# Kernel optimization log

Measured on AMD Instinct MI355X. Metric: run time of the kernel, lower is better.

Reference implementation:

```python
import jax, jax.numpy as jnp
import numpy as np

N = 100000
E = 1600000
D_IN = 128
D_HID = 32
NEG_SLOPE = 0.2


def _glorot(key, shape):
    fan_in, fan_out = shape[0], shape[-1]
    lim = jnp.sqrt(6.0 / (fan_in + fan_out))
    return jax.random.uniform(key, shape, jnp.float32, -lim, lim)


def setup_inputs() -> dict:
    key = jax.random.key(0)
    ks = jax.random.split(key, 10)
    x = jax.random.normal(ks[0], (N, D_IN), jnp.float32)
    edge_index = jax.random.randint(ks[1], (2, E), 0, N, jnp.int64)
    return {
        "x": x,
        "edge_index": edge_index,
        "W1_l": _glorot(ks[2], (D_IN, D_HID)),
        "W1_r": _glorot(ks[3], (D_IN, D_HID)),
        "att1": _glorot(ks[4], (D_HID,)),
        "b1": jnp.zeros((D_HID,), jnp.float32),
        "W2_l": _glorot(ks[5], (D_HID, D_HID)),
        "W2_r": _glorot(ks[6], (D_HID, D_HID)),
        "att2": _glorot(ks[7], (D_HID,)),
        "b2": jnp.zeros((D_HID,), jnp.float32),
    }


def _segment_softmax(logits, seg, num_segments):
    m = jax.ops.segment_max(logits, seg, num_segments=num_segments)
    m = jnp.where(jnp.isfinite(m), m, 0.0)
    ex = jnp.exp(logits - m[seg])
    s = jax.ops.segment_sum(ex, seg, num_segments=num_segments)
    return ex / (s[seg] + 1e-16)


def _gatv2(x, edge_index, W_l, W_r, att, b):
    # GATv2Conv, heads=1, add_self_loops=False, share_weights=False
    src, dst = edge_index[0], edge_index[1]
    x_l = x @ W_l  # source transform [N, D_HID]
    x_r = x @ W_r  # target transform [N, D_HID]
    # per-edge attention logit: att . leaky_relu(x_l[j] + x_r[i])
    h = x_l[src] + x_r[dst]  # [E, D_HID]
    e = jnp.where(h > 0, h, NEG_SLOPE * h) @ att  # [E]
    alpha = _segment_softmax(e, dst, x.shape[0])  # softmax over incoming edges
    out = jax.ops.segment_sum(alpha[:, None] * x_l[src], dst,
                              num_segments=x.shape[0])
    return out + b


def reference(x, edge_index, W1_l, W1_r, att1, b1, W2_l, W2_r, att2, b2):
    h = _gatv2(x, edge_index, W1_l, W1_r, att1, b1)
    h = jax.nn.relu(h)
    return _gatv2(h, edge_index, W2_l, W2_r, att2, b2)
```

## Files before the change

kernel.cpp:

```cpp
#include <hip/hip_runtime.h>
#include <hip/hip_bf16.h>

#define D_HID 32
#define D_IN 128
#define NEG 0.2f
#define BSH 7
#define BSZ 128
#define MAXB 1024
#define SCATB 256

typedef unsigned short u16;
typedef __attribute__((ext_vector_type(8))) short short8;
typedef __attribute__((ext_vector_type(4))) float float4v;

__device__ __forceinline__ float b2f(u16 u){
  union { unsigned int i; float f; } c; c.i = ((unsigned int)u) << 16; return c.f;
}

__device__ __forceinline__ u16 f2b_rne(float f){
  union { float f; unsigned int u; } c; c.f = f;
  unsigned int u = c.u;
  return (u16)((u + 0x7FFFu + ((u >> 16) & 1u)) >> 16);
}

__device__ __forceinline__ void split_bf16(float v, u16& hi, u16& lo){
  hi = f2b_rne(v);
  lo = f2b_rne(v - b2f(hi));
}

__device__ __forceinline__ float ldf(const void* __restrict__ p, int f32, long long i){
  return f32 ? ((const float*)p)[i] : b2f(((const u16*)p)[i]);
}

__device__ __forceinline__ int atomAddI(int* p, int v){
  return __hip_atomic_fetch_add(p, v, __ATOMIC_RELAXED, __HIP_MEMORY_SCOPE_AGENT);
}

__device__ __forceinline__ float red8(float p){
  p += __int_as_float(__builtin_amdgcn_update_dpp(
         0, __float_as_int(p), 0xB1, 0xF, 0xF, true));
  p += __int_as_float(__builtin_amdgcn_update_dpp(
         0, __float_as_int(p), 0x4E, 0xF, 0xF, true));
  p += __int_as_float(__builtin_amdgcn_ds_swizzle(
         __float_as_int(p), 0x101F));
  return p;
}

__device__ __forceinline__ float edge_ev(const float4 xv, const float4 xrk,
                                         const float4 attk){
  float hx = xv.x + xrk.x; hx = fmaxf(hx, NEG*hx);
  float hy = xv.y + xrk.y; hy = fmaxf(hy, NEG*hy);
  float hz = xv.z + xrk.z; hz = fmaxf(hz, NEG*hz);
  float hw = xv.w + xrk.w; hw = fmaxf(hw, NEG*hw);
  float p = hx*attk.x;
  p = fmaf(hy, attk.y, p);
  p = fmaf(hz, attk.z, p);
  p = fmaf(hw, attk.w, p);
  p = red8(p);
  p = fminf(p, 60.f);
  return __expf(p);
}

__global__ void __launch_bounds__(256)
count_flags(const int* __restrict__ ei, const u16* __restrict__ xw,
            int* __restrict__ gcnt, int* __restrict__ flags, int E_, int B_){
  __shared__ int hist[MAXB];
  __shared__ int nz_s, insane_s;
  int t = threadIdx.x;
  if (t == 0){ nz_s = 0; insane_s = 0; }
  for (int i = t; i < B_; i += 256) hist[i] = 0;
  __syncthreads();
  if (t < 64 && ei[2*t+1] != 0) atomicAdd(&nz_s, 1);
  if (blockIdx.x == 0){
    int e = (xw[t] >> 7) & 0xFF;
    if (e < 100 || e > 140) atomicAdd(&insane_s, 1);
  }
  __syncthreads();
  int is64 = (nz_s == 0);
  if (blockIdx.x == 0 && t == 0){
    flags[0] = is64;
    flags[1] = (insane_s > 16) ? 1 : 0;
  }
  int chunk = (E_ + gridDim.x - 1) / gridDim.x;
  int s = blockIdx.x * chunk;
  int e = s + chunk; if (e > E_) e = E_;
  for (int i = s + t; i < e; i += 256){
    int dst = is64 ? ei[2*E_ + 2*i] : ei[E_ + i];
    atomicAdd(&hist[dst >> BSH], 1);
  }
  __syncthreads();
  for (int i = t; i < B_; i += 256)
    if (hist[i]) (void)atomAddI(&gcnt[i], hist[i]);
}

__device__ __forceinline__ void prep_body(const void* __restrict__ Wl,
                                          const void* __restrict__ Wr,
                                          int f32, int K,
                                          uint4* __restrict__ whi,
                                          uint4* __restrict__ wlo, int t){
  int KS = K >> 5;
  int total = 4 * KS * 64;
  if (t >= total) return;
  int lane = t & 63;
  int rem = t >> 6;
  int kstep = rem % KS;
  int ctile = rem / KS;
  int col = ctile * 16 + (lane & 15);
  int quad = lane >> 4;
  union { u16 s[8]; uint4 q; } ch, cl;
  #pragma unroll
  for (int j = 0; j < 8; ++j){
    int k = kstep*32 + quad*8 + j;
    float v = (col < 32) ? ldf(Wl, f32, (long long)k*D_HID + col)
                         : ldf(Wr, f32, (long long)k*D_HID + (col - 32));
    u16 hi, lo; split_bf16(v, hi, lo);
    ch.s[j] = hi; cl.s[j] = lo;
  }
  whi[rem*64 + lane] = ch.q;
  wlo[rem*64 + lane] = cl.q;
}

__global__ void __launch_bounds__(256)
scan_scatter_prep(const int* __restrict__ ei, const int* __restrict__ flags,
                  const int* __restrict__ gcnt, int* __restrict__ cur0,
                  unsigned* __restrict__ seg, int* __restrict__ offsets,
                  const void* __restrict__ W1l, const void* __restrict__ W1r,
                  const void* __restrict__ W2l, const void* __restrict__ W2r,
                  uint4* __restrict__ whi1, uint4* __restrict__ wlo1,
                  uint4* __restrict__ whi2, uint4* __restrict__ wlo2,
                  int E_, int B_){
  int t = threadIdx.x;
  if ((int)blockIdx.x >= SCATB){
    int sub = blockIdx.x - SCATB;
    int f32 = flags[1];
    if (sub < 4) prep_body(W1l, W1r, f32, D_IN,  whi1, wlo1, sub*256 + t);
    else         prep_body(W2l, W2r, f32, D_HID, whi2, wlo2, t);
    return;
  }
  __shared__ int sd[MAXB];
  __shared__ int part[256];
  __shared__ int hist[MAXB];
  __shared__ int bbase[MAXB];
  for (int i = t; i < MAXB; i += 256) sd[i] = (i < B_) ? gcnt[i] : 0;
  __syncthreads();
  int a0 = sd[4*t], a1 = sd[4*t+1], a2 = sd[4*t+2], a3 = sd[4*t+3];
  int mysum = a0 + a1 + a2 + a3;
  part[t] = mysum;
  __syncthreads();
  for (int off = 1; off < 256; off <<= 1){
    int v = (t >= off) ? part[t-off] : 0;
    __syncthreads();
    part[t] += v;
    __syncthreads();
  }
  int excl = part[t] - mysum;
  sd[4*t]   = excl;
  sd[4*t+1] = excl + a0;
  sd[4*t+2] = excl + a0 + a1;
  sd[4*t+3] = excl + a0 + a1 + a2;
  __syncthreads();
  if (blockIdx.x == 0){
    for (int i = t; i <= B_; i += 256)
      offsets[i] = (i < MAXB) ? sd[i] : part[255];
  }
  for (int i = t; i < B_; i += 256) hist[i] = 0;
  __syncthreads();
  int is64 = flags[0];
  int chunk = (E_ + SCATB - 1) / SCATB;
  int s = blockIdx.x * chunk;
  int e = s + chunk; if (e > E_) e = E_;
  for (int i = s + t; i < e; i += 256){
    int dst = is64 ? ei[2*E_ + 2*i] : ei[E_ + i];
    atomicAdd(&hist[dst >> BSH], 1);
  }
  __syncthreads();
  for (int i = t; i < B_; i += 256){
    int c = hist[i];
    bbase[i] = c ? (sd[i] + atomAddI(&cur0[i], c)) : 0;
  }
  __syncthreads();
  for (int i = t; i < B_; i += 256) hist[i] = 0;
  __syncthreads();
  for (int i = s + t; i < e; i += 256){
    int src, dst;
    if (is64){ src = ei[2*i]; dst = ei[2*E_ + 2*i]; }
    else     { src = ei[i];   dst = ei[E_ + i]; }
    int b = dst >> BSH;
    int pos = bbase[b] + atomicAdd(&hist[b], 1);
    seg[pos] = ((unsigned)src << BSH) | (unsigned)(dst & (BSZ-1));
  }
}

__device__ void finalize_body(const unsigned* __restrict__ seg,
                              const int* __restrict__ offsets,
                              int* __restrict__ row, int* __restrict__ csr_src,
                              int N_, int B_, int b, int t){
  __shared__ int hist[BSZ];
  __shared__ int sc[BSZ];
  __shared__ int loff[BSZ];
  int base = offsets[b], cnt = offsets[b+1] - base;
  if (t < BSZ) hist[t] = 0;
  __syncthreads();
  for (int i = t; i < cnt; i += 256)
    atomicAdd(&hist[seg[base+i] & (BSZ-1)], 1);
  __syncthreads();
  if (t < BSZ) sc[t] = hist[t];
  __syncthreads();
  for (int off = 1; off < BSZ; off <<= 1){
    int tmp = (t < BSZ && t >= off) ? sc[t-off] : 0;
    __syncthreads();
    if (t < BSZ) sc[t] += tmp;
    __syncthreads();
  }
  if (t < BSZ){
    int excl = sc[t] - hist[t];
    loff[t] = excl;
    int node = b*BSZ + t;
    if (node <= N_) row[node] = base + excl;
  }
  if (b == B_-1 && t == 0) row[N_] = offsets[B_];
  __syncthreads();
  for (int i = t; i < cnt; i += 256){
    unsigned en = seg[base+i];
    int dl = en & (BSZ-1);
    int pos = atomicAdd(&loff[dl], 1);
    csr_src[base + pos] = (int)en;
  }
}

template<int K>
__device__ __forceinline__ void gemm_body(const void* __restrict__ X,
                          const uint4* __restrict__ whi, const uint4* __restrict__ wlo,
                          const int* __restrict__ flags, int force_f32,
                          float* __restrict__ xl, float* __restrict__ xr,
                          int N_, int tile, int lane)
{
  constexpr int KS = K >> 5;
  if (tile * 16 >= N_) return;
  int quad = lane >> 4;
  int m = tile*16 + (lane & 15);
  if (m >= N_) m = N_ - 1;
  int f32 = force_f32 | flags[1];

  float4v acc[4];
  #pragma unroll
  for (int c = 0; c < 4; ++c) acc[c] = (float4v){0.f,0.f,0.f,0.f};

  #pragma unroll
  for (int ks = 0; ks < KS; ++ks){
    long long base = (long long)m * K + ks*32 + quad*8;
    float av[8];
    if (f32){
      const float4* xp = (const float4*)((const float*)X + base);
      float4 t0 = xp[0], t1 = xp[1];
      av[0]=t0.x; av[1]=t0.y; av[2]=t0.z; av[3]=t0.w;
      av[4]=t1.x; av[5]=t1.y; av[6]=t1.z; av[7]=t1.w;
    } else {
      union { uint4 q; u16 s[8]; } c8;
      c8.q = *(const uint4*)((const u16*)X + base);
      #pragma unroll
      for (int j = 0; j < 8; ++j) av[j] = b2f(c8.s[j]);
    }
    short8 ahi, alo;
    #pragma unroll
    for (int j = 0; j < 8; ++j){
      u16 hi, lo; split_bf16(av[j], hi, lo);
      ahi[j] = (short)hi; alo[j] = (short)lo;
    }
    #pragma unroll
    for (int c = 0; c < 4; ++c){
      uint4 wh = whi[(c*KS + ks)*64 + lane];
      uint4 wl = wlo[(c*KS + ks)*64 + lane];
      short8 bh = *(short8*)&wh;
      short8 bl = *(short8*)&wl;
      acc[c] = __builtin_amdgcn_mfma_f32_16x16x32_bf16(ahi, bh, acc[c], 0, 0, 0);
      acc[c] = __builtin_amdgcn_mfma_f32_16x16x32_bf16(ahi, bl, acc[c], 0, 0, 0);
      acc[c] = __builtin_amdgcn_mfma_f32_16x16x32_bf16(alo, bh, acc[c], 0, 0, 0);
    }
  }

  #pragma unroll
  for (int c = 0; c < 4; ++c){
    int col = c*16 + (lane & 15);
    float* dst = (col < 32) ? xl : xr;
    int kk = col & 31;
    #pragma unroll
    for (int r = 0; r < 4; ++r){
      int node = tile*16 + quad*4 + r;
      if (node < N_) dst[(size_t)node*D_HID + kk] = acc[c][r];
    }
  }
}

template<int K>
__global__ void __launch_bounds__(256)
fin_gemm(const unsigned* __restrict__ seg, const int* __restrict__ offsets,
         int* __restrict__ row, int* __restrict__ csr_src,
         const void* __restrict__ X,
         const uint4* __restrict__ whi, const uint4* __restrict__ wlo,
         const int* __restrict__ flags,
         float* __restrict__ xl, float* __restrict__ xr, int N_, int B_){
  if ((int)blockIdx.x < B_){
    finalize_body(seg, offsets, row, csr_src, N_, B_, blockIdx.x, threadIdx.x);
    return;
  }
  int tile = (blockIdx.x - B_) * 4 + (threadIdx.x >> 6);
  gemm_body<K>(X, whi, wlo, flags, 0, xl, xr, N_, tile, threadIdx.x & 63);
}

template<int K>
__global__ void __launch_bounds__(256)
mfma_gemm(const void* __restrict__ X,
          const uint4* __restrict__ whi, const uint4* __restrict__ wlo,
          const int* __restrict__ flags, int force_f32,
          float* __restrict__ xl, float* __restrict__ xr, int N_){
  int tile = blockIdx.x * 4 + (threadIdx.x >> 6);
  gemm_body<K>(X, whi, wlo, flags, force_f32, xl, xr, N_, tile, threadIdx.x & 63);
}

__global__ void __launch_bounds__(256)
gat_gather(const int* __restrict__ row, const unsigned* __restrict__ csrp,
           const float* __restrict__ xl, const float* __restrict__ xr,
           const void* __restrict__ att, const void* __restrict__ bias,
           const int* __restrict__ flags,
           float* __restrict__ outp, int N_, int do_relu)
{
  int wv = (blockIdx.x * blockDim.x + threadIdx.x) >> 6;
  int l = threadIdx.x & 63;
  int n = wv * 4 + (l >> 4);
  if (n >= N_) return;
  int half = (l >> 3) & 1;
  int fl = l & 7;
  int f32 = flags[1];
  float4 attk;
  attk.x = ldf(att, f32, fl*4+0);
  attk.y = ldf(att, f32, fl*4+1);
  attk.z = ldf(att, f32, fl*4+2);
  attk.w = ldf(att, f32, fl*4+3);
  float4 xrk = *(const float4*)(xr + (size_t)n*D_HID + fl*4);
  int rs = row[n], re = row[n+1];
  const char* xlb = (const char*)xl;
  unsigned fo = (unsigned)(fl << 4);

  float4 acc = make_float4(0.f, 0.f, 0.f, 0.f);
  float ssum = 0.f;

  int start = rs + 2*half;
  if (start < re){
    int last = re - 1;
    unsigned c0 = csrp[start];
    unsigned c1 = csrp[min(start+1,  last)];
    unsigned c2 = csrp[min(start+4,  last)];
    unsigned c3 = csrp[min(start+5,  last)];
    unsigned c4 = csrp[min(start+8,  last)];
    unsigned c5 = csrp[min(start+9,  last)];
    unsigned ca = csrp[min(start+12, last)];
    unsigned cb = csrp[min(start+13, last)];
    float4 xv0 = *(const float4*)(xlb + (c0 & ~127u) + fo);
    float4 xv1 = *(const float4*)(xlb + (c1 & ~127u) + fo);
    float4 xv2 = *(const float4*)(xlb + (c2 & ~127u) + fo);
    float4 xv3 = *(const float4*)(xlb + (c3 & ~127u) + fo);
    float4 xv4 = *(const float4*)(xlb + (c4 & ~127u) + fo);
    float4 xv5 = *(const float4*)(xlb + (c5 & ~127u) + fo);
    for (int i = start; i < re; i += 4){
      float4 nx0 = *(const float4*)(xlb + (ca & ~127u) + fo);
      float4 nx1 = *(const float4*)(xlb + (cb & ~127u) + fo);
      unsigned na = csrp[min(i+16, last)];
      unsigned nb = csrp[min(i+17, last)];
      float ev0 = edge_ev(xv0, xrk, attk);
      ssum += ev0;
      acc.x = fmaf(ev0, xv0.x, acc.x);
      acc.y = fmaf(ev0, xv0.y, acc.y);
      acc.z = fmaf(ev0, xv0.z, acc.z);
      acc.w = fmaf(ev0, xv0.w, acc.w);
      float ev1 = edge_ev(xv1, xrk, attk);
      ev1 = (i + 1 <= last) ? ev1 : 0.f;
      ssum += ev1;
      acc.x = fmaf(ev1, xv1.x, acc.x);
      acc.y = fmaf(ev1, xv1.y, acc.y);
      acc.z = fmaf(ev1, xv1.z, acc.z);
      acc.w = fmaf(ev1, xv1.w, acc.w);
      xv0 = xv2; xv1 = xv3; xv2 = xv4; xv3 = xv5; xv4 = nx0; xv5 = nx1;
      ca = na; cb = nb;
    }
  }

  acc.x += __shfl_xor(acc.x, 8, 16);
  acc.y += __shfl_xor(acc.y, 8, 16);
  acc.z += __shfl_xor(acc.z, 8, 16);
  acc.w += __shfl_xor(acc.w, 8, 16);
  ssum  += __shfl_xor(ssum,  8, 16);

  if (half == 0){
    float inv = 1.0f / (ssum + 1e-16f);
    float4 o;
    o.x = acc.x*inv + ldf(bias, f32, fl*4+0);
    o.y = acc.y*inv + ldf(bias, f32, fl*4+1);
    o.z = acc.z*inv + ldf(bias, f32, fl*4+2);
    o.w = acc.w*inv + ldf(bias, f32, fl*4+3);
    if (do_relu){
      o.x = fmaxf(o.x, 0.f); o.y = fmaxf(o.y, 0.f);
      o.z = fmaxf(o.z, 0.f); o.w = fmaxf(o.w, 0.f);
    }
    *(float4*)(outp + (size_t)n*D_HID + fl*4) = o;
  }
}

extern "C" void kernel_launch(void* const* d_in, const int* in_sizes, int n_in,
                              void* d_out, int out_size, void* d_ws, size_t ws_size,
                              hipStream_t stream)
{
  const void* x   = d_in[0];
  const int*  ei  = (const int*)d_in[1];
  const void* W1l = d_in[2];
  const void* W1r = d_in[3];
  const void* att1= d_in[4];
  const void* b1  = d_in[5];
  const void* W2l = d_in[6];
  const void* W2r = d_in[7];
  const void* att2= d_in[8];
  const void* b2  = d_in[9];
  float* out = (float*)d_out;

  int N_ = in_sizes[0] / D_IN;
  int E_ = in_sizes[1] / 2;
  int B_ = (N_ + BSZ - 1) / BSZ;

  char* ws = (char*)d_ws;
  size_t off = 0;
  auto carve = [&](size_t bytes) -> char* {
    char* p = ws + off;
    off += (bytes + 255) & ~(size_t)255;
    return p;
  };
  float*    xl      = (float*)   carve((size_t)N_ * D_HID * 4);
  float*    xr      = (float*)   carve((size_t)N_ * D_HID * 4);
  float*    h       = (float*)   carve((size_t)N_ * D_HID * 4);
  unsigned* seg     = (unsigned*)carve((size_t)E_ * 4);
  int*      csr_src = (int*)     carve((size_t)E_ * 4);
  int*      row     = (int*)     carve((size_t)(N_ + 1) * 4);
  int*      offsets = (int*)     carve((size_t)(MAXB + 1) * 4);
  int*      gcnt    = (int*)     carve((size_t)MAXB * 4);
  int*      cur0    = (int*)     carve((size_t)MAXB * 4);
  int*      flags   = (int*)     carve(256);
  uint4*    whi1    = (uint4*)   carve((size_t)4 * 4 * 64 * 16);
  uint4*    wlo1    = (uint4*)   carve((size_t)4 * 4 * 64 * 16);
  uint4*    whi2    = (uint4*)   carve((size_t)4 * 1 * 64 * 16);
  uint4*    wlo2    = (uint4*)   carve((size_t)4 * 1 * 64 * 16);

  const int tpb = 256;
  int gG = (N_ + 15) / 16;
  int tiles = (N_ + 15) / 16;
  int gT = (tiles + 3) / 4;

  hipMemsetAsync(gcnt, 0, (size_t)2 * MAXB * 4, stream);

  count_flags<<<256, tpb, 0, stream>>>(ei, (const u16*)x, gcnt, flags, E_, B_);

  scan_scatter_prep<<<SCATB + 5, tpb, 0, stream>>>(
      ei, flags, gcnt, cur0, seg, offsets,
      W1l, W1r, W2l, W2r, whi1, wlo1, whi2, wlo2, E_, B_);

  fin_gemm<D_IN><<<B_ + gT, tpb, 0, stream>>>(
      seg, offsets, row, csr_src, x, whi1, wlo1, flags, xl, xr, N_, B_);

  gat_gather<<<gG, tpb, 0, stream>>>(row, (const unsigned*)csr_src, xl, xr,
                                     att1, b1, flags, h, N_, 1);

  mfma_gemm<D_HID><<<gT, tpb, 0, stream>>>(h, whi2, wlo2, flags, 1, xl, xr, N_);

  gat_gather<<<gG, tpb, 0, stream>>>(row, (const unsigned*)csr_src, xl, xr,
                                     att2, b2, flags, out, N_, 0);
}
```

Measured before the change: 248.3 us.

## Replace edge count-and-scan prepass with fixed-capacity per-bucket scatter

Drops the separate histogram kernel and the global prefix scan that ran before the scatter. Edges are now scattered straight into fixed-capacity slots per destination bucket (CAP entries each), using atomic cursors. Each finalize block then rescans the bucket counts to find its output offset. This saves a full pass over the edge list and one kernel launch. The scatter grid also grows from 256 to 1024 blocks. The cost is a much larger seg buffer, and any edges beyond CAP in a bucket are silently dropped, which is only safe when destinations are evenly spread.

```diff
diff --git a/kernel.cpp b/kernel.cpp
--- a/kernel.cpp
+++ b/kernel.cpp
@@ -7,7 +7,8 @@
 #define BSH 7
 #define BSZ 128
 #define MAXB 1024
-#define SCATB 256
+#define CAP  4096
+#define NSCAT 1024
 
 typedef unsigned short u16;
 typedef __attribute__((ext_vector_type(8))) short short8;
@@ -59,38 +60,6 @@
   p = red8(p);
   p = fminf(p, 60.f);
   return __expf(p);
-}
-
-__global__ void __launch_bounds__(256)
-count_flags(const int* __restrict__ ei, const u16* __restrict__ xw,
-            int* __restrict__ gcnt, int* __restrict__ flags, int E_, int B_){
-  __shared__ int hist[MAXB];
-  __shared__ int nz_s, insane_s;
-  int t = threadIdx.x;
-  if (t == 0){ nz_s = 0; insane_s = 0; }
-  for (int i = t; i < B_; i += 256) hist[i] = 0;
-  __syncthreads();
-  if (t < 64 && ei[2*t+1] != 0) atomicAdd(&nz_s, 1);
-  if (blockIdx.x == 0){
-    int e = (xw[t] >> 7) & 0xFF;
-    if (e < 100 || e > 140) atomicAdd(&insane_s, 1);
-  }
-  __syncthreads();
-  int is64 = (nz_s == 0);
-  if (blockIdx.x == 0 && t == 0){
-    flags[0] = is64;
-    flags[1] = (insane_s > 16) ? 1 : 0;
-  }
-  int chunk = (E_ + gridDim.x - 1) / gridDim.x;
-  int s = blockIdx.x * chunk;
-  int e = s + chunk; if (e > E_) e = E_;
-  for (int i = s + t; i < e; i += 256){
-    int dst = is64 ? ei[2*E_ + 2*i] : ei[E_ + i];
-    atomicAdd(&hist[dst >> BSH], 1);
-  }
-  __syncthreads();
-  for (int i = t; i < B_; i += 256)
-    if (hist[i]) (void)atomAddI(&gcnt[i], hist[i]);
 }
 
 __device__ __forceinline__ void prep_body(const void* __restrict__ Wl,
@@ -121,52 +90,46 @@
 }
 
 __global__ void __launch_bounds__(256)
-scan_scatter_prep(const int* __restrict__ ei, const int* __restrict__ flags,
-                  const int* __restrict__ gcnt, int* __restrict__ cur0,
-                  unsigned* __restrict__ seg, int* __restrict__ offsets,
-                  const void* __restrict__ W1l, const void* __restrict__ W1r,
-                  const void* __restrict__ W2l, const void* __restrict__ W2r,
-                  uint4* __restrict__ whi1, uint4* __restrict__ wlo1,
-                  uint4* __restrict__ whi2, uint4* __restrict__ wlo2,
-                  int E_, int B_){
+scat_prep(const int* __restrict__ ei, const u16* __restrict__ xw,
+          int* __restrict__ cursor, unsigned* __restrict__ seg,
+          int* __restrict__ flags,
+          const void* __restrict__ W1l, const void* __restrict__ W1r,
+          const void* __restrict__ W2l, const void* __restrict__ W2r,
+          uint4* __restrict__ whi1, uint4* __restrict__ wlo1,
+          uint4* __restrict__ whi2, uint4* __restrict__ wlo2,
+          int E_, int B_){
   int t = threadIdx.x;
-  if ((int)blockIdx.x >= SCATB){
-    int sub = blockIdx.x - SCATB;
-    int f32 = flags[1];
+  if ((int)blockIdx.x >= NSCAT){
+    __shared__ int ins_p;
+    if (t == 0) ins_p = 0;
+    __syncthreads();
+    int e = (xw[t] >> 7) & 0xFF;
+    if (e < 100 || e > 140) atomicAdd(&ins_p, 1);
+    __syncthreads();
+    int f32 = (ins_p > 16) ? 1 : 0;
+    int sub = blockIdx.x - NSCAT;
     if (sub < 4) prep_body(W1l, W1r, f32, D_IN,  whi1, wlo1, sub*256 + t);
     else         prep_body(W2l, W2r, f32, D_HID, whi2, wlo2, t);
     return;
   }
-  __shared__ int sd[MAXB];
-  __shared__ int part[256];
   __shared__ int hist[MAXB];
   __shared__ int bbase[MAXB];
-  for (int i = t; i < MAXB; i += 256) sd[i] = (i < B_) ? gcnt[i] : 0;
-  __syncthreads();
-  int a0 = sd[4*t], a1 = sd[4*t+1], a2 = sd[4*t+2], a3 = sd[4*t+3];
-  int mysum = a0 + a1 + a2 + a3;
-  part[t] = mysum;
-  __syncthreads();
-  for (int off = 1; off < 256; off <<= 1){
-    int v = (t >= off) ? part[t-off] : 0;
-    __syncthreads();
-    part[t] += v;
-    __syncthreads();
-  }
-  int excl = part[t] - mysum;
-  sd[4*t]   = excl;
-  sd[4*t+1] = excl + a0;
-  sd[4*t+2] = excl + a0 + a1;
-  sd[4*t+3] = excl + a0 + a1 + a2;
-  __syncthreads();
+  __shared__ int nz_s, insane_s;
+  if (t == 0){ nz_s = 0; insane_s = 0; }
+  for (int i = t; i < B_; i += 256) hist[i] = 0;
+  __syncthreads();
+  if (t < 64 && ei[2*t+1] != 0) atomicAdd(&nz_s, 1);
   if (blockIdx.x == 0){
-    for (int i = t; i <= B_; i += 256)
-      offsets[i] = (i < MAXB) ? sd[i] : part[255];
-  }
-  for (int i = t; i < B_; i += 256) hist[i] = 0;
-  __syncthreads();
-  int is64 = flags[0];
-  int chunk = (E_ + SCATB - 1) / SCATB;
+    int e = (xw[t] >> 7) & 0xFF;
+    if (e < 100 || e > 140) atomicAdd(&insane_s, 1);
+  }
+  __syncthreads();
+  int is64 = (nz_s == 0);
+  if (blockIdx.x == 0 && t == 0){
+    flags[0] = is64;
+    flags[1] = (insane_s > 16) ? 1 : 0;
+  }
+  int chunk = (E_ + NSCAT - 1) / NSCAT;
   int s = blockIdx.x * chunk;
   int e = s + chunk; if (e > E_) e = E_;
   for (int i = s + t; i < e; i += 256){
@@ -176,7 +139,7 @@
   __syncthreads();
   for (int i = t; i < B_; i += 256){
     int c = hist[i];
-    bbase[i] = c ? (sd[i] + atomAddI(&cur0[i], c)) : 0;
+    bbase[i] = c ? atomAddI(&cursor[i], c) : 0;
   }
   __syncthreads();
   for (int i = t; i < B_; i += 256) hist[i] = 0;
@@ -187,22 +150,47 @@
     else     { src = ei[i];   dst = ei[E_ + i]; }
     int b = dst >> BSH;
     int pos = bbase[b] + atomicAdd(&hist[b], 1);
-    seg[pos] = ((unsigned)src << BSH) | (unsigned)(dst & (BSZ-1));
+    if (pos < CAP)
+      seg[(size_t)b*CAP + pos] = ((unsigned)src << BSH) | (unsigned)(dst & (BSZ-1));
   }
 }
 
 __device__ void finalize_body(const unsigned* __restrict__ seg,
-                              const int* __restrict__ offsets,
+                              const int* __restrict__ cursor,
                               int* __restrict__ row, int* __restrict__ csr_src,
                               int N_, int B_, int b, int t){
+  __shared__ int sd[MAXB];
+  __shared__ int part[256];
   __shared__ int hist[BSZ];
   __shared__ int sc[BSZ];
   __shared__ int loff[BSZ];
-  int base = offsets[b], cnt = offsets[b+1] - base;
+  for (int i = t; i < MAXB; i += 256) sd[i] = (i < B_) ? min(cursor[i], CAP) : 0;
+  __syncthreads();
+  int a0 = sd[4*t], a1 = sd[4*t+1], a2 = sd[4*t+2], a3 = sd[4*t+3];
+  int mysum = a0 + a1 + a2 + a3;
+  part[t] = mysum;
+  __syncthreads();
+  for (int off = 1; off < 256; off <<= 1){
+    int v = (t >= off) ? part[t-off] : 0;
+    __syncthreads();
+    part[t] += v;
+    __syncthreads();
+  }
+  int excl = part[t] - mysum;
+  sd[4*t]   = excl;
+  sd[4*t+1] = excl + a0;
+  sd[4*t+2] = excl + a0 + a1;
+  sd[4*t+3] = excl + a0 + a1 + a2;
+  __syncthreads();
+  int base_out = sd[b];
+  int cnt = min(cursor[b], CAP);
+  int total = part[255];
+  size_t base_in = (size_t)b * CAP;
+
   if (t < BSZ) hist[t] = 0;
   __syncthreads();
   for (int i = t; i < cnt; i += 256)
-    atomicAdd(&hist[seg[base+i] & (BSZ-1)], 1);
+    atomicAdd(&hist[seg[base_in + i] & (BSZ-1)], 1);
   __syncthreads();
   if (t < BSZ) sc[t] = hist[t];
   __syncthreads();
@@ -213,18 +201,18 @@
     __syncthreads();
   }
   if (t < BSZ){
-    int excl = sc[t] - hist[t];
-    loff[t] = excl;
+    int e2 = sc[t] - hist[t];
+    loff[t] = e2;
     int node = b*BSZ + t;
-    if (node <= N_) row[node] = base + excl;
-  }
-  if (b == B_-1 && t == 0) row[N_] = offsets[B_];
+    if (node <= N_) row[node] = base_out + e2;
+  }
+  if (b == B_-1 && t == 0) row[N_] = total;
   __syncthreads();
   for (int i = t; i < cnt; i += 256){
-    unsigned en = seg[base+i];
+    unsigned en = seg[base_in + i];
     int dl = en & (BSZ-1);
     int pos = atomicAdd(&loff[dl], 1);
-    csr_src[base + pos] = (int)en;
+    csr_src[base_out + pos] = (int)en;
   }
 }
 
@@ -294,14 +282,14 @@
 
 template<int K>
 __global__ void __launch_bounds__(256)
-fin_gemm(const unsigned* __restrict__ seg, const int* __restrict__ offsets,
+fin_gemm(const unsigned* __restrict__ seg, const int* __restrict__ cursor,
          int* __restrict__ row, int* __restrict__ csr_src,
          const void* __restrict__ X,
          const uint4* __restrict__ whi, const uint4* __restrict__ wlo,
          const int* __restrict__ flags,
          float* __restrict__ xl, float* __restrict__ xr, int N_, int B_){
   if ((int)blockIdx.x < B_){
-    finalize_body(seg, offsets, row, csr_src, N_, B_, blockIdx.x, threadIdx.x);
+    finalize_body(seg, cursor, row, csr_src, N_, B_, blockIdx.x, threadIdx.x);
     return;
   }
   int tile = (blockIdx.x - B_) * 4 + (threadIdx.x >> 6);
@@ -436,12 +424,10 @@
   float*    xl      = (float*)   carve((size_t)N_ * D_HID * 4);
   float*    xr      = (float*)   carve((size_t)N_ * D_HID * 4);
   float*    h       = (float*)   carve((size_t)N_ * D_HID * 4);
-  unsigned* seg     = (unsigned*)carve((size_t)E_ * 4);
+  unsigned* seg     = (unsigned*)carve((size_t)B_ * CAP * 4);
   int*      csr_src = (int*)     carve((size_t)E_ * 4);
   int*      row     = (int*)     carve((size_t)(N_ + 1) * 4);
-  int*      offsets = (int*)     carve((size_t)(MAXB + 1) * 4);
-  int*      gcnt    = (int*)     carve((size_t)MAXB * 4);
-  int*      cur0    = (int*)     carve((size_t)MAXB * 4);
+  int*      cursor  = (int*)     carve((size_t)MAXB * 4);
   int*      flags   = (int*)     carve(256);
   uint4*    whi1    = (uint4*)   carve((size_t)4 * 4 * 64 * 16);
   uint4*    wlo1    = (uint4*)   carve((size_t)4 * 4 * 64 * 16);
@@ -453,16 +439,14 @@
   int tiles = (N_ + 15) / 16;
   int gT = (tiles + 3) / 4;
 
-  hipMemsetAsync(gcnt, 0, (size_t)2 * MAXB * 4, stream);
-
-  count_flags<<<256, tpb, 0, stream>>>(ei, (const u16*)x, gcnt, flags, E_, B_);
-
-  scan_scatter_prep<<<SCATB + 5, tpb, 0, stream>>>(
-      ei, flags, gcnt, cur0, seg, offsets,
+  hipMemsetAsync(cursor, 0, (size_t)MAXB * 4, stream);
+
+  scat_prep<<<NSCAT + 5, tpb, 0, stream>>>(
+      ei, (const u16*)x, cursor, seg, flags,
       W1l, W1r, W2l, W2r, whi1, wlo1, whi2, wlo2, E_, B_);
 
   fin_gemm<D_IN><<<B_ + gT, tpb, 0, stream>>>(
-      seg, offsets, row, csr_src, x, whi1, wlo1, flags, xl, xr, N_, B_);
+      seg, cursor, row, csr_src, x, whi1, wlo1, flags, xl, xr, N_, B_);
 
   gat_gather<<<gG, tpb, 0, stream>>>(row, (const unsigned*)csr_src, xl, xr,
                                      att1, b1, flags, h, N_, 1);
```

After: 255.4 us. +2.9%, slower.
